# Kernel optimization log

Hardware: AMD Instinct MI355X
Metric: run time of the kernel (lower is better)

The kernel has to match this reference:

```python
import jax, jax.numpy as jnp
import numpy as np

LOSS1_COEFF = 1.0
LOSS2_COEFF = 1.0
LOSS3_COEFF = 1.0
LOSS4_COEFF = 0.5


def smooth_l1(x, y):
    # torch smooth_l1_loss, beta=1, reduction='mean'
    d = jnp.abs(x - y)
    return jnp.mean(jnp.where(d < 1.0, 0.5 * d * d, d - 0.5))


def setup_inputs() -> dict:
    key = jax.random.key(0)
    k1, k2 = jax.random.split(key)
    B, N, F = 256, 8192, 13
    targets = jax.random.uniform(k1, (B, N, F), dtype=jnp.float32)
    preds = jax.random.uniform(k2, (B, N, F), dtype=jnp.float32)
    return {"targets": targets, "preds": preds}


def reference(targets, preds):
    tb = targets[:, :, :4]  # [B,N,4]
    pb = preds[:, :, :4]
    # The original builds a [B,N,N] pairwise IoU matrix and takes its diagonal;
    # the diagonal is exactly the elementwise matched-pair IoU, computed here directly.
    xx1 = jnp.maximum(tb[..., 0], pb[..., 0])
    yy1 = jnp.maximum(tb[..., 1], pb[..., 1])
    xx2 = jnp.minimum(tb[..., 2], pb[..., 2])
    yy2 = jnp.minimum(tb[..., 3], pb[..., 3])
    w = jnp.clip(xx2 - xx1, 0.0)
    h = jnp.clip(yy2 - yy1, 0.0)
    inter = w * h
    area1 = (tb[..., 2] - tb[..., 0]) * (tb[..., 3] - tb[..., 1])
    area2 = (pb[..., 2] - pb[..., 0]) * (pb[..., 3] - pb[..., 1])
    ious = inter / (area1 + area2 - inter + 1e-07)  # [B,N]

    loss1 = smooth_l1(jnp.ones_like(ious), ious)
    loss2 = smooth_l1(tb, pb)
    loss3 = smooth_l1(targets[:, :, -1], preds[:, :, -1])
    loss4 = smooth_l1(targets[:, :, 4:12], preds[:, :, 4:12])
    return (LOSS1_COEFF * loss1 + LOSS2_COEFF * loss2
            + LOSS3_COEFF * loss3 + LOSS4_COEFF * loss4)
```

## Files before the change

kernel.cpp:

```cpp
#include <hip/hip_runtime.h>
#include <hip/hip_bf16.h>


#define ROWS_TOTAL   (256 * 8192)
#define ROWS_PER_BLK 1024
#define NBLK         (ROWS_TOTAL / ROWS_PER_BLK)
#define F4_PER_BLK   (ROWS_PER_BLK * 13 / 4)

#define W1 (1.0f / 2097152.0f)
#define W2 (1.0f / 8388608.0f)
#define W3 (1.0f / 2097152.0f)
#define W4 (1.0f / 33554432.0f)

__device__ __forceinline__ float sl1(float d) {
    d = fabsf(d);
    return d < 1.0f ? 0.5f * d * d : d - 0.5f;
}

__global__ __launch_bounds__(256) void loss_stage1(const float* __restrict__ T,
                                                   const float* __restrict__ P,
                                                   float* __restrict__ partial) {
    __shared__ float wred[4];
    const int tid = threadIdx.x;
    const int blk = blockIdx.x;

    float acc = 0.0f;

    {
        const float4* t4 = (const float4*)T + (long long)blk * F4_PER_BLK;
        const float4* p4 = (const float4*)P + (long long)blk * F4_PER_BLK;
        const unsigned ebase = (unsigned)blk * (F4_PER_BLK * 4u);
#pragma unroll
        for (int k = 0; k < 13; ++k) {
            const int i = k * 256 + tid;
            float4 a = t4[i];
            float4 b = p4[i];
            unsigned f0 = (ebase + 4u * (unsigned)i) % 13u;
            const float da[4] = {a.x - b.x, a.y - b.y, a.z - b.z, a.w - b.w};
#pragma unroll
            for (int j = 0; j < 4; ++j) {
                unsigned f = f0 + (unsigned)j;
                if (f >= 13u) f -= 13u;
                float w = (f < 4u) ? W2 : ((f == 12u) ? W3 : W4);
                acc += w * sl1(da[j]);
            }
        }
    }

    {
#pragma unroll
        for (int k = 0; k < 4; ++k) {
            const long long r = (long long)blk * ROWS_PER_BLK + k * 256 + tid;
            const float* tr = T + r * 13;
            const float* pr = P + r * 13;
            float t0 = tr[0], t1 = tr[1], t2 = tr[2], t3 = tr[3];
            float p0 = pr[0], p1 = pr[1], p2 = pr[2], p3 = pr[3];

            float w = fmaxf(fminf(t2, p2) - fmaxf(t0, p0), 0.0f);
            float h = fmaxf(fminf(t3, p3) - fmaxf(t1, p1), 0.0f);
            float inter = w * h;
            float a1 = (t2 - t0) * (t3 - t1);
            float a2 = (p2 - p0) * (p3 - p1);
            float u  = a1 + a2 - inter + 1e-7f;
            float iou = inter * __builtin_amdgcn_rcpf(u);
            acc += W1 * sl1(1.0f - iou);
        }
    }

#pragma unroll
    for (int off = 32; off > 0; off >>= 1)
        acc += __shfl_down(acc, off, 64);
    if ((tid & 63) == 0) wred[tid >> 6] = acc;
    __syncthreads();
    if (tid == 0)
        partial[blk] = wred[0] + wred[1] + wred[2] + wred[3];
}

__global__ __launch_bounds__(256) void loss_stage2(const float* __restrict__ partial,
                                                   float* __restrict__ out) {
    __shared__ float wred[4];
    const int tid = threadIdx.x;
    float a = 0.0f;
#pragma unroll
    for (int k = 0; k < NBLK / 256; ++k) a += partial[k * 256 + tid];
#pragma unroll
    for (int off = 32; off > 0; off >>= 1)
        a += __shfl_down(a, off, 64);
    if ((tid & 63) == 0) wred[tid >> 6] = a;
    __syncthreads();
    if (tid == 0) out[0] = wred[0] + wred[1] + wred[2] + wred[3];
}

extern "C" void kernel_launch(void* const* d_in, const int* in_sizes, int n_in,
                              void* d_out, int out_size, void* d_ws, size_t ws_size,
                              hipStream_t stream) {
    const float* targets = (const float*)d_in[0];
    const float* preds   = (const float*)d_in[1];
    float* out     = (float*)d_out;
    float* partial = (float*)d_ws;

    loss_stage1<<<NBLK, 256, 0, stream>>>(targets, preds, partial);
    loss_stage2<<<1, 256, 0, stream>>>(partial, out);
}
```

Before: 242.7 us.

## Stage box columns in LDS instead of re-reading global for IoU

The IoU pass now reads the four box coordinates from shared memory, which is filled during the coalesced float4 streaming pass. This replaces the second set of strided global loads, which are likely L2 hits but cost latency and cache bandwidth. Blocks shrink to 128 threads covering 512 rows, which doubles the partial count to 4096, and the field-index modulo is precomputed per thread. The trade-offs are extra LDS stores under divergent branches, a block barrier, and an exact divide in place of the rcp builtin.

```diff
diff --git a/kernel.cpp b/kernel.cpp
--- a/kernel.cpp
+++ b/kernel.cpp
@@ -2,10 +2,11 @@
 #include <hip/hip_bf16.h>
 
 
-#define ROWS_TOTAL   (256 * 8192)
-#define ROWS_PER_BLK 1024
-#define NBLK         (ROWS_TOTAL / ROWS_PER_BLK)
-#define F4_PER_BLK   (ROWS_PER_BLK * 13 / 4)
+#define ROWS_TOTAL (256 * 8192)
+#define TPB        128
+#define RPB        512
+#define NBLK       (ROWS_TOTAL / RPB)
+#define F4PB       (RPB * 13 / 4)
 
 #define W1 (1.0f / 2097152.0f)
 #define W2 (1.0f / 8388608.0f)
@@ -17,54 +18,65 @@
     return d < 1.0f ? 0.5f * d * d : d - 0.5f;
 }
 
-__global__ __launch_bounds__(256) void loss_stage1(const float* __restrict__ T,
-                                                   const float* __restrict__ P,
-                                                   float* __restrict__ partial) {
-    __shared__ float wred[4];
+__global__ __launch_bounds__(TPB, 4) void loss_stage1(const float* __restrict__ T,
+                                                      const float* __restrict__ P,
+                                                      float* __restrict__ partial) {
+    __shared__ float stT[RPB * 4];
+    __shared__ float stP[RPB * 4];
+    __shared__ float wred[2];
+
     const int tid = threadIdx.x;
     const int blk = blockIdx.x;
 
+    const float4* t4 = (const float4*)T + (long long)blk * F4PB;
+    const float4* p4 = (const float4*)P + (long long)blk * F4PB;
+
+    const unsigned ftid = (4u * (unsigned)tid) % 13u;
+
     float acc = 0.0f;
 
-    {
-        const float4* t4 = (const float4*)T + (long long)blk * F4_PER_BLK;
-        const float4* p4 = (const float4*)P + (long long)blk * F4_PER_BLK;
-        const unsigned ebase = (unsigned)blk * (F4_PER_BLK * 4u);
 #pragma unroll
-        for (int k = 0; k < 13; ++k) {
-            const int i = k * 256 + tid;
-            float4 a = t4[i];
-            float4 b = p4[i];
-            unsigned f0 = (ebase + 4u * (unsigned)i) % 13u;
-            const float da[4] = {a.x - b.x, a.y - b.y, a.z - b.z, a.w - b.w};
+    for (int k = 0; k < 13; ++k) {
+        const int i = k * TPB + tid;
+        float4 a = t4[i];
+        float4 b = p4[i];
+
+        const unsigned e0   = 4u * (unsigned)i;
+        unsigned       f0   = ftid + (unsigned)((512 * k) % 13);
+        if (f0 >= 13u) f0 -= 13u;
+        const unsigned row0 = e0 / 13u;
+
+        const float av[4] = {a.x, a.y, a.z, a.w};
+        const float bv[4] = {b.x, b.y, b.z, b.w};
 #pragma unroll
-            for (int j = 0; j < 4; ++j) {
-                unsigned f = f0 + (unsigned)j;
-                if (f >= 13u) f -= 13u;
-                float w = (f < 4u) ? W2 : ((f == 12u) ? W3 : W4);
-                acc += w * sl1(da[j]);
+        for (int j = 0; j < 4; ++j) {
+            unsigned f   = f0 + (unsigned)j;
+            unsigned row = row0;
+            if (f >= 13u) { f -= 13u; row += 1u; }
+            float w = (f < 4u) ? W2 : ((f == 12u) ? W3 : W4);
+            acc += w * sl1(av[j] - bv[j]);
+            if (f < 4u) {
+                stT[row * 4u + f] = av[j];
+                stP[row * 4u + f] = bv[j];
             }
         }
     }
 
-    {
+    __syncthreads();
+
 #pragma unroll
-        for (int k = 0; k < 4; ++k) {
-            const long long r = (long long)blk * ROWS_PER_BLK + k * 256 + tid;
-            const float* tr = T + r * 13;
-            const float* pr = P + r * 13;
-            float t0 = tr[0], t1 = tr[1], t2 = tr[2], t3 = tr[3];
-            float p0 = pr[0], p1 = pr[1], p2 = pr[2], p3 = pr[3];
+    for (int k = 0; k < 4; ++k) {
+        const int r = k * TPB + tid;
+        float4 tb = ((const float4*)stT)[r];
+        float4 pb = ((const float4*)stP)[r];
 
-            float w = fmaxf(fminf(t2, p2) - fmaxf(t0, p0), 0.0f);
-            float h = fmaxf(fminf(t3, p3) - fmaxf(t1, p1), 0.0f);
-            float inter = w * h;
-            float a1 = (t2 - t0) * (t3 - t1);
-            float a2 = (p2 - p0) * (p3 - p1);
-            float u  = a1 + a2 - inter + 1e-7f;
-            float iou = inter * __builtin_amdgcn_rcpf(u);
-            acc += W1 * sl1(1.0f - iou);
-        }
+        float w = fmaxf(fminf(tb.z, pb.z) - fmaxf(tb.x, pb.x), 0.0f);
+        float h = fmaxf(fminf(tb.w, pb.w) - fmaxf(tb.y, pb.y), 0.0f);
+        float inter = w * h;
+        float a1 = (tb.z - tb.x) * (tb.w - tb.y);
+        float a2 = (pb.z - pb.x) * (pb.w - pb.y);
+        float iou = inter / (a1 + a2 - inter + 1e-7f);
+        acc += W1 * sl1(1.0f - iou);
     }
 
 #pragma unroll
@@ -73,7 +85,7 @@
     if ((tid & 63) == 0) wred[tid >> 6] = acc;
     __syncthreads();
     if (tid == 0)
-        partial[blk] = wred[0] + wred[1] + wred[2] + wred[3];
+        partial[blk] = wred[0] + wred[1];
 }
 
 __global__ __launch_bounds__(256) void loss_stage2(const float* __restrict__ partial,
@@ -99,6 +111,6 @@
     float* out     = (float*)d_out;
     float* partial = (float*)d_ws;
 
-    loss_stage1<<<NBLK, 256, 0, stream>>>(targets, preds, partial);
+    loss_stage1<<<NBLK, TPB, 0, stream>>>(targets, preds, partial);
     loss_stage2<<<1, 256, 0, stream>>>(partial, out);
 }
```

Result: slower. 280.9 us (+15.7%).

## Stream rows through per-wave double-buffered LDS via direct global-to-LDS loads

Applied to the files above, without the earlier changes.

Replaces the block-wide float4 pass plus the separate IoU re-read with a persistent-style kernel of 512 blocks. Each wavefront owns a contiguous run of rows and streams them through a double-buffered LDS staging area using global_load_lds, with waitcnt-based pipelining. Each lane then computes all four losses for one row from LDS, so the box fields are no longer read twice and the per-element modulo-13 weight logic goes away. The cost is dword-granularity loads, strided LDS reads that may cause bank conflicts, hand-encoded waitcnt constants, and fewer blocks in flight.

```diff
diff --git a/kernel.cpp b/kernel.cpp
--- a/kernel.cpp
+++ b/kernel.cpp
@@ -2,78 +2,99 @@
 #include <hip/hip_bf16.h>
 
 
-#define ROWS_TOTAL   (256 * 8192)
-#define ROWS_PER_BLK 1024
-#define NBLK         (ROWS_TOTAL / ROWS_PER_BLK)
-#define F4_PER_BLK   (ROWS_PER_BLK * 13 / 4)
+#define ROWS_TOTAL   (1 << 21)
+#define TPB          256
+#define WPB          4
+#define NBLK         512
+#define NSTREAM      (NBLK * WPB)
+#define ROWS_STREAM  (ROWS_TOTAL / NSTREAM)
+#define ROWS_STAGE   64
+#define NSTAGE       (ROWS_STREAM / ROWS_STAGE)
+#define FLT_STAGE    (ROWS_STAGE * 13)
+
+#define WAIT_VM26    0x4F7A
+#define WAIT_VM0     0x0F70
 
 #define W1 (1.0f / 2097152.0f)
 #define W2 (1.0f / 8388608.0f)
 #define W3 (1.0f / 2097152.0f)
 #define W4 (1.0f / 33554432.0f)
 
+typedef const __attribute__((address_space(1))) float gfloat;
+typedef __attribute__((address_space(3))) float lfloat;
+
 __device__ __forceinline__ float sl1(float d) {
     d = fabsf(d);
     return d < 1.0f ? 0.5f * d * d : d - 0.5f;
 }
 
-__global__ __launch_bounds__(256) void loss_stage1(const float* __restrict__ T,
+__global__ __launch_bounds__(TPB) void loss_stage1(const float* __restrict__ T,
                                                    const float* __restrict__ P,
                                                    float* __restrict__ partial) {
-    __shared__ float wred[4];
-    const int tid = threadIdx.x;
-    const int blk = blockIdx.x;
+    __shared__ float lds[WPB][2][2][FLT_STAGE];
+
+    const int tid  = threadIdx.x;
+    const int lane = tid & 63;
+    const int wv   = tid >> 6;
+    const int sid  = blockIdx.x * WPB + wv;
+    const long long base13 = (long long)sid * ROWS_STREAM * 13;
+
+    auto issue = [&](int s, int b) {
+        const float* tg = T + base13 + (long long)s * FLT_STAGE + lane;
+        const float* pg = P + base13 + (long long)s * FLT_STAGE + lane;
+        lfloat* lt = (lfloat*)&lds[wv][b][0][0];
+        lfloat* lp = (lfloat*)&lds[wv][b][1][0];
+#pragma unroll
+        for (int i = 0; i < 13; ++i) {
+            __builtin_amdgcn_global_load_lds((gfloat*)(tg + i * 64), lt + i * 64, 4, 0, 0);
+            __builtin_amdgcn_global_load_lds((gfloat*)(pg + i * 64), lp + i * 64, 4, 0, 0);
+        }
+    };
 
     float acc = 0.0f;
+    auto consume = [&](int b) {
+        const float* t = &lds[wv][b][0][lane * 13];
+        const float* p = &lds[wv][b][1][lane * 13];
 
-    {
-        const float4* t4 = (const float4*)T + (long long)blk * F4_PER_BLK;
-        const float4* p4 = (const float4*)P + (long long)blk * F4_PER_BLK;
-        const unsigned ebase = (unsigned)blk * (F4_PER_BLK * 4u);
+        float t0 = t[0], t1 = t[1], t2 = t[2], t3 = t[3];
+        float p0 = p[0], p1 = p[1], p2 = p[2], p3 = p[3];
+
+        float s2 = sl1(t0 - p0) + sl1(t1 - p1) + sl1(t2 - p2) + sl1(t3 - p3);
+
+        float s4 = 0.0f;
 #pragma unroll
-        for (int k = 0; k < 13; ++k) {
-            const int i = k * 256 + tid;
-            float4 a = t4[i];
-            float4 b = p4[i];
-            unsigned f0 = (ebase + 4u * (unsigned)i) % 13u;
-            const float da[4] = {a.x - b.x, a.y - b.y, a.z - b.z, a.w - b.w};
-#pragma unroll
-            for (int j = 0; j < 4; ++j) {
-                unsigned f = f0 + (unsigned)j;
-                if (f >= 13u) f -= 13u;
-                float w = (f < 4u) ? W2 : ((f == 12u) ? W3 : W4);
-                acc += w * sl1(da[j]);
-            }
-        }
+        for (int f = 4; f < 12; ++f) s4 += sl1(t[f] - p[f]);
+
+        float s3 = sl1(t[12] - p[12]);
+
+        float w = fmaxf(fminf(t2, p2) - fmaxf(t0, p0), 0.0f);
+        float h = fmaxf(fminf(t3, p3) - fmaxf(t1, p1), 0.0f);
+        float inter = w * h;
+        float a1 = (t2 - t0) * (t3 - t1);
+        float a2 = (p2 - p0) * (p3 - p1);
+        float iou = inter / (a1 + a2 - inter + 1e-7f);
+
+        acc += W1 * sl1(1.0f - iou) + W2 * s2 + W3 * s3 + W4 * s4;
+    };
+
+    issue(0, 0);
+    issue(1, 1);
+
+#pragma unroll 1
+    for (int s = 0; s < NSTAGE - 1; ++s) {
+        __builtin_amdgcn_s_waitcnt(WAIT_VM26);
+        asm volatile("" ::: "memory");
+        consume(s & 1);
+        if (s < NSTAGE - 2) issue(s + 2, s & 1);
     }
-
-    {
-#pragma unroll
-        for (int k = 0; k < 4; ++k) {
-            const long long r = (long long)blk * ROWS_PER_BLK + k * 256 + tid;
-            const float* tr = T + r * 13;
-            const float* pr = P + r * 13;
-            float t0 = tr[0], t1 = tr[1], t2 = tr[2], t3 = tr[3];
-            float p0 = pr[0], p1 = pr[1], p2 = pr[2], p3 = pr[3];
-
-            float w = fmaxf(fminf(t2, p2) - fmaxf(t0, p0), 0.0f);
-            float h = fmaxf(fminf(t3, p3) - fmaxf(t1, p1), 0.0f);
-            float inter = w * h;
-            float a1 = (t2 - t0) * (t3 - t1);
-            float a2 = (p2 - p0) * (p3 - p1);
-            float u  = a1 + a2 - inter + 1e-7f;
-            float iou = inter * __builtin_amdgcn_rcpf(u);
-            acc += W1 * sl1(1.0f - iou);
-        }
-    }
+    __builtin_amdgcn_s_waitcnt(WAIT_VM0);
+    asm volatile("" ::: "memory");
+    consume((NSTAGE - 1) & 1);
 
 #pragma unroll
     for (int off = 32; off > 0; off >>= 1)
         acc += __shfl_down(acc, off, 64);
-    if ((tid & 63) == 0) wred[tid >> 6] = acc;
-    __syncthreads();
-    if (tid == 0)
-        partial[blk] = wred[0] + wred[1] + wred[2] + wred[3];
+    if (lane == 0) partial[sid] = acc;
 }
 
 __global__ __launch_bounds__(256) void loss_stage2(const float* __restrict__ partial,
@@ -82,7 +103,7 @@
     const int tid = threadIdx.x;
     float a = 0.0f;
 #pragma unroll
-    for (int k = 0; k < NBLK / 256; ++k) a += partial[k * 256 + tid];
+    for (int k = 0; k < NSTREAM / 256; ++k) a += partial[k * 256 + tid];
 #pragma unroll
     for (int off = 32; off > 0; off >>= 1)
         a += __shfl_down(a, off, 64);
@@ -99,6 +120,6 @@
     float* out     = (float*)d_out;
     float* partial = (float*)d_ws;
 
-    loss_stage1<<<NBLK, 256, 0, stream>>>(targets, preds, partial);
+    loss_stage1<<<NBLK, TPB, 0, stream>>>(targets, preds, partial);
     loss_stage2<<<1, 256, 0, stream>>>(partial, out);
 }
```

Measured after the change: 234.4 us. -3.4%, faster.

## Load each thread's four rows into registers and reuse them for IoU

Applied to the files above, without the earlier changes.

Each thread now loads four consecutive rows of targets and preds as 13 float4 into registers. It computes all smooth-L1 terms with compile-time weights and the IoU term from the same registers, avoiding the second scalar read of the box columns and the per-element modulo. The cost is a strided per-lane access pattern (208-byte stride) that is less coalesced, plus higher register use. IoU now uses true division instead of the fast reciprocal.

```diff
diff --git a/kernel.cpp b/kernel.cpp
--- a/kernel.cpp
+++ b/kernel.cpp
@@ -2,10 +2,8 @@
 #include <hip/hip_bf16.h>
 
 
-#define ROWS_TOTAL   (256 * 8192)
-#define ROWS_PER_BLK 1024
-#define NBLK         (ROWS_TOTAL / ROWS_PER_BLK)
-#define F4_PER_BLK   (ROWS_PER_BLK * 13 / 4)
+#define NBLK 2048
+#define TPB  256
 
 #define W1 (1.0f / 2097152.0f)
 #define W2 (1.0f / 8388608.0f)
@@ -17,54 +15,49 @@
     return d < 1.0f ? 0.5f * d * d : d - 0.5f;
 }
 
-__global__ __launch_bounds__(256) void loss_stage1(const float* __restrict__ T,
-                                                   const float* __restrict__ P,
-                                                   float* __restrict__ partial) {
+__global__ __launch_bounds__(TPB, 2) void loss_stage1(const float* __restrict__ T,
+                                                      const float* __restrict__ P,
+                                                      float* __restrict__ partial) {
     __shared__ float wred[4];
-    const int tid = threadIdx.x;
-    const int blk = blockIdx.x;
+
+    const int tid  = threadIdx.x;
+    const long long sb = (long long)blockIdx.x * TPB + tid;
+
+    const float4* __restrict__ t4 = (const float4*)(T + sb * 52);
+    const float4* __restrict__ p4 = (const float4*)(P + sb * 52);
+
+    float4 tv4[13], pv4[13];
+#pragma unroll
+    for (int k = 0; k < 13; ++k) tv4[k] = t4[k];
+#pragma unroll
+    for (int k = 0; k < 13; ++k) pv4[k] = p4[k];
+
+    const float* tv = (const float*)tv4;
+    const float* pv = (const float*)pv4;
 
     float acc = 0.0f;
 
-    {
-        const float4* t4 = (const float4*)T + (long long)blk * F4_PER_BLK;
-        const float4* p4 = (const float4*)P + (long long)blk * F4_PER_BLK;
-        const unsigned ebase = (unsigned)blk * (F4_PER_BLK * 4u);
 #pragma unroll
-        for (int k = 0; k < 13; ++k) {
-            const int i = k * 256 + tid;
-            float4 a = t4[i];
-            float4 b = p4[i];
-            unsigned f0 = (ebase + 4u * (unsigned)i) % 13u;
-            const float da[4] = {a.x - b.x, a.y - b.y, a.z - b.z, a.w - b.w};
-#pragma unroll
-            for (int j = 0; j < 4; ++j) {
-                unsigned f = f0 + (unsigned)j;
-                if (f >= 13u) f -= 13u;
-                float w = (f < 4u) ? W2 : ((f == 12u) ? W3 : W4);
-                acc += w * sl1(da[j]);
-            }
-        }
+    for (int e = 0; e < 52; ++e) {
+        constexpr_weight:;
+        const int f = e % 13;
+        const float w = (f < 4) ? W2 : ((f == 12) ? W3 : W4);
+        acc += w * sl1(tv[e] - pv[e]);
     }
 
-    {
 #pragma unroll
-        for (int k = 0; k < 4; ++k) {
-            const long long r = (long long)blk * ROWS_PER_BLK + k * 256 + tid;
-            const float* tr = T + r * 13;
-            const float* pr = P + r * 13;
-            float t0 = tr[0], t1 = tr[1], t2 = tr[2], t3 = tr[3];
-            float p0 = pr[0], p1 = pr[1], p2 = pr[2], p3 = pr[3];
+    for (int r = 0; r < 4; ++r) {
+        const int b = r * 13;
+        float t0 = tv[b+0], t1 = tv[b+1], t2 = tv[b+2], t3 = tv[b+3];
+        float p0 = pv[b+0], p1 = pv[b+1], p2 = pv[b+2], p3 = pv[b+3];
 
-            float w = fmaxf(fminf(t2, p2) - fmaxf(t0, p0), 0.0f);
-            float h = fmaxf(fminf(t3, p3) - fmaxf(t1, p1), 0.0f);
-            float inter = w * h;
-            float a1 = (t2 - t0) * (t3 - t1);
-            float a2 = (p2 - p0) * (p3 - p1);
-            float u  = a1 + a2 - inter + 1e-7f;
-            float iou = inter * __builtin_amdgcn_rcpf(u);
-            acc += W1 * sl1(1.0f - iou);
-        }
+        float w = fmaxf(fminf(t2, p2) - fmaxf(t0, p0), 0.0f);
+        float h = fmaxf(fminf(t3, p3) - fmaxf(t1, p1), 0.0f);
+        float inter = w * h;
+        float a1 = (t2 - t0) * (t3 - t1);
+        float a2 = (p2 - p0) * (p3 - p1);
+        float iou = inter / (a1 + a2 - inter + 1e-7f);
+        acc += W1 * sl1(1.0f - iou);
     }
 
 #pragma unroll
@@ -73,7 +66,7 @@
     if ((tid & 63) == 0) wred[tid >> 6] = acc;
     __syncthreads();
     if (tid == 0)
-        partial[blk] = wred[0] + wred[1] + wred[2] + wred[3];
+        partial[blockIdx.x] = wred[0] + wred[1] + wred[2] + wred[3];
 }
 
 __global__ __launch_bounds__(256) void loss_stage2(const float* __restrict__ partial,
@@ -99,6 +92,6 @@
     float* out     = (float*)d_out;
     float* partial = (float*)d_ws;
 
-    loss_stage1<<<NBLK, 256, 0, stream>>>(targets, preds, partial);
+    loss_stage1<<<NBLK, TPB, 0, stream>>>(targets, preds, partial);
     loss_stage2<<<1, 256, 0, stream>>>(partial, out);
 }
```

New measurement: 237.5 us. -2.2%, faster.
